# Performance work log

Measured on AMD Instinct MI355X. Metric: run time of the kernel, lower is better.

The kernel has to match this reference:

```python
import jax, jax.numpy as jnp
import numpy as np

BITS = 32
N = 2_000_000

# Soft logic gates on {0,1}-valued floats (matching the SNN gate modules)
# xor(a,b) = a + b - 2ab ; not(x) = 1 - x ; and(a,b) = a*b ; or(a,b) = a + b - ab

def setup_inputs() -> dict:
    key = jax.random.key(0)
    kA, kB = jax.random.split(key)
    A = jax.random.randint(kA, (N, BITS), 0, 2).astype(jnp.float32)
    B = jax.random.randint(kB, (N, BITS), 0, 2).astype(jnp.float32)
    return {"A": A, "B": B}


def reference(A, B):
    # A, B: [..., bits], MSB first, values in {0,1}
    xor_all = A + B - 2.0 * A * B          # VecXOR
    eq_all = 1.0 - xor_all                  # VecNOT(xor)
    not_b = 1.0 - B                         # VecNOT(B)
    gt_all = A * not_b                      # VecAND -> A_i AND (NOT B_i)

    # a_eq_b: AND-tree over all bits
    a_eq_b = jnp.prod(eq_all, axis=-1, keepdims=True)

    # eq_prefix_i = AND of eq[0..i-1]; prefix_0 = 1 (no constraint for MSB)
    eq_cum = jnp.cumprod(eq_all, axis=-1)                      # [..., bits]
    prefix = jnp.concatenate(
        [jnp.ones_like(eq_cum[..., :1]), eq_cum[..., :-1]], axis=-1
    )                                                          # [..., bits]

    # term_i = prefix_i AND gt_i ; a_gt_b = OR over i of term_i
    # chained soft-OR of binary terms == 1 - prod(1 - term_i)
    terms = prefix * gt_all
    a_gt_b = 1.0 - jnp.prod(1.0 - terms, axis=-1, keepdims=True)

    return (a_gt_b, a_eq_b)
```

## Files before the change

### kernel.cpp

```cpp
#include <hip/hip_runtime.h>
#include <hip/hip_bf16.h>


__global__ void __launch_bounds__(256)
comparator_kernel(const float* __restrict__ A, const float* __restrict__ B,
                  float* __restrict__ out_gt, float* __restrict__ out_eq, int n) {
    int row = blockIdx.x * blockDim.x + threadIdx.x;
    if (row >= n) return;

    const float4* a4 = reinterpret_cast<const float4*>(A) + (size_t)row * 8;
    const float4* b4 = reinterpret_cast<const float4*>(B) + (size_t)row * 8;

    unsigned int abits = 0, bbits = 0;
#pragma unroll
    for (int j = 0; j < 8; ++j) {
        float4 a = a4[j];
        float4 b = b4[j];
        abits = (abits << 4) |
                ((unsigned)(a.x > 0.5f) << 3) | ((unsigned)(a.y > 0.5f) << 2) |
                ((unsigned)(a.z > 0.5f) << 1) | ((unsigned)(a.w > 0.5f));
        bbits = (bbits << 4) |
                ((unsigned)(b.x > 0.5f) << 3) | ((unsigned)(b.y > 0.5f) << 2) |
                ((unsigned)(b.z > 0.5f) << 1) | ((unsigned)(b.w > 0.5f));
    }

    out_gt[row] = (abits > bbits) ? 1.0f : 0.0f;
    out_eq[row] = (abits == bbits) ? 1.0f : 0.0f;
}

extern "C" void kernel_launch(void* const* d_in, const int* in_sizes, int n_in,
                              void* d_out, int out_size, void* d_ws, size_t ws_size,
                              hipStream_t stream) {
    const float* A = (const float*)d_in[0];
    const float* B = (const float*)d_in[1];
    float* out = (float*)d_out;

    const int BITS = 32;
    int n = in_sizes[0] / BITS;

    float* out_gt = out;
    float* out_eq = out + n;

    int block = 256;
    int grid = (n + block - 1) / block;
    comparator_kernel<<<grid, block, 0, stream>>>(A, B, out_gt, out_eq, n);
}
```

Baseline: 506.1 us.

## Coalesce loads by assigning one float4 per thread with shuffle reduction

Each row's 32 floats are now split across 8 lanes, one float4 per lane, so consecutive lanes read consecutive 16-byte chunks and the loads coalesce fully. Before, each thread read 128 contiguous bytes with a per-thread stride. The nibbles are combined with three xor-shuffles and lane 0 of each group writes the result. This launches eight times as many threads and adds shuffle work, and only one lane in eight does the store.

```diff
diff --git a/kernel.cpp b/kernel.cpp
--- a/kernel.cpp
+++ b/kernel.cpp
@@ -4,28 +4,35 @@
 
 __global__ void __launch_bounds__(256)
 comparator_kernel(const float* __restrict__ A, const float* __restrict__ B,
-                  float* __restrict__ out_gt, float* __restrict__ out_eq, int n) {
-    int row = blockIdx.x * blockDim.x + threadIdx.x;
-    if (row >= n) return;
+                  float* __restrict__ out_gt, float* __restrict__ out_eq,
+                  long long n) {
+    long long tid = (long long)blockIdx.x * blockDim.x + threadIdx.x;
+    long long totalVec = n * 8;
+    if (tid >= totalVec) return;
 
-    const float4* a4 = reinterpret_cast<const float4*>(A) + (size_t)row * 8;
-    const float4* b4 = reinterpret_cast<const float4*>(B) + (size_t)row * 8;
+    const float4* a4 = reinterpret_cast<const float4*>(A);
+    const float4* b4 = reinterpret_cast<const float4*>(B);
+    float4 a = a4[tid];
+    float4 b = b4[tid];
 
-    unsigned int abits = 0, bbits = 0;
-#pragma unroll
-    for (int j = 0; j < 8; ++j) {
-        float4 a = a4[j];
-        float4 b = b4[j];
-        abits = (abits << 4) |
-                ((unsigned)(a.x > 0.5f) << 3) | ((unsigned)(a.y > 0.5f) << 2) |
-                ((unsigned)(a.z > 0.5f) << 1) | ((unsigned)(a.w > 0.5f));
-        bbits = (bbits << 4) |
-                ((unsigned)(b.x > 0.5f) << 3) | ((unsigned)(b.y > 0.5f) << 2) |
-                ((unsigned)(b.z > 0.5f) << 1) | ((unsigned)(b.w > 0.5f));
+    unsigned an = ((unsigned)(a.x > 0.5f) << 3) | ((unsigned)(a.y > 0.5f) << 2) |
+                  ((unsigned)(a.z > 0.5f) << 1) |  (unsigned)(a.w > 0.5f);
+    unsigned bn = ((unsigned)(b.x > 0.5f) << 3) | ((unsigned)(b.y > 0.5f) << 2) |
+                  ((unsigned)(b.z > 0.5f) << 1) |  (unsigned)(b.w > 0.5f);
+
+    int nib = (int)(tid & 7);
+    unsigned av = an << (4 * (7 - nib));
+    unsigned bv = bn << (4 * (7 - nib));
+
+    av |= __shfl_xor((int)av, 1, 64); bv |= __shfl_xor((int)bv, 1, 64);
+    av |= __shfl_xor((int)av, 2, 64); bv |= __shfl_xor((int)bv, 2, 64);
+    av |= __shfl_xor((int)av, 4, 64); bv |= __shfl_xor((int)bv, 4, 64);
+
+    if (nib == 0) {
+        long long row = tid >> 3;
+        out_gt[row] = (av > bv)  ? 1.0f : 0.0f;
+        out_eq[row] = (av == bv) ? 1.0f : 0.0f;
     }
-
-    out_gt[row] = (abits > bbits) ? 1.0f : 0.0f;
-    out_eq[row] = (abits == bbits) ? 1.0f : 0.0f;
 }
 
 extern "C" void kernel_launch(void* const* d_in, const int* in_sizes, int n_in,
@@ -36,12 +43,13 @@
     float* out = (float*)d_out;
 
     const int BITS = 32;
-    int n = in_sizes[0] / BITS;
+    long long n = in_sizes[0] / BITS;
 
     float* out_gt = out;
     float* out_eq = out + n;
 
+    long long totalVec = n * 8;
     int block = 256;
-    int grid = (n + block - 1) / block;
-    comparator_kernel<<<grid, block, 0, stream>>>(A, B, out_gt, out_eq, n);
+    long long grid = (totalVec + block - 1) / block;
+    comparator_kernel<<<(int)grid, block, 0, stream>>>(A, B, out_gt, out_eq, n);
 }
```

New measurement: 469.7 us. -7.2%, faster.
